# Kernel tuning notes

Hardware: AMD Instinct MI355X
Metric: run time of the kernel (lower is better)

Reference implementation:

```python
import jax, jax.numpy as jnp
import numpy as np

D = 1024
B, N = 4, 2048

def setup_inputs() -> dict:
    key = jax.random.key(0)
    ks = jax.random.split(key, 7)
    sc = 1.0 / np.sqrt(D)
    return {
        "x": jax.random.normal(ks[0], (B, N, D), dtype=jnp.float32),
        "wq_w": jax.random.normal(ks[1], (D, D), dtype=jnp.float32) * sc,
        "wq_b": jax.random.normal(ks[2], (D,), dtype=jnp.float32) * 0.01,
        "wk_w": jax.random.normal(ks[3], (D, D), dtype=jnp.float32) * sc,
        "wk_b": jax.random.normal(ks[4], (D,), dtype=jnp.float32) * 0.01,
        "wv_w": jax.random.normal(ks[5], (D, D), dtype=jnp.float32) * sc,
        "wv_b": jax.random.normal(ks[6], (D,), dtype=jnp.float32) * 0.01,
    }

def reference(x, wq_w, wq_b, wk_w, wk_b, wv_w, wv_b):
    # torch Linear: y = x @ W^T + b
    q = x @ wq_w.T + wq_b
    k = x @ wk_w.T + wk_b
    v = x @ wv_w.T + wv_b
    d = q.shape[-1]
    s = jnp.einsum("bid,bjd->bij", q, k) / jnp.sqrt(jnp.float32(d))
    # faithful to original: triu then transpose (zeros, NOT -inf, enter the softmax)
    t = jnp.swapaxes(jnp.triu(s), -2, -1)
    p = jax.nn.softmax(t, axis=-2)
    attn = jnp.swapaxes(jnp.triu(p), -2, -1) @ v
    return attn
```

## Files before the change

kernel.cpp:

```cpp
#include <hip/hip_runtime.h>
#include <hip/hip_fp16.h>
#include <cstdint>

typedef _Float16 half8_t __attribute__((ext_vector_type(8)));
typedef float f32x4 __attribute__((ext_vector_type(4)));

#define D_ 1024
#define B_ 4
#define N_ 2048
#define M_ (B_*N_)
#define NC_ 3072

#define OFF_WCAT  0u
#define OFF_BCAT  6291456u
#define OFF_XB    6303744u
#define OFF_Q     23080960u
#define OFF_K     39858176u
#define OFF_V     56635392u
#define OFF_ZP    73412608u
#define OFF_DEXP  74461184u
#define OFF_SV    74493952u
#define OFF_INVD  74756096u
#define OFF_CD    74788864u

__device__ __forceinline__ void gload_lds16(const void* g, void* l) {
  __builtin_amdgcn_global_load_lds(
      (const __attribute__((address_space(1))) unsigned int*)(uintptr_t)g,
      (__attribute__((address_space(3))) unsigned int*)(uintptr_t)l, 16, 0, 0);
}

__device__ __forceinline__ void stage128x64(const __half* rowbase, char* lds, int tid) {
#pragma unroll
  for (int inst = 0; inst < 4; ++inst) {
    int L  = inst * 4096 + tid * 16;
    int r  = L >> 7;
    int cb = L & 127;
    int cbs = cb ^ ((r & 7) << 4);
    gload_lds16((const char*)rowbase + (size_t)r * (D_ * 2) + cbs, lds + L);
  }
}

__device__ __forceinline__ half8_t ldsfrag(const char* lds, int row, int cbyte) {
  int b = (row << 7) + (cbyte ^ ((row & 7) << 4));
  return *reinterpret_cast<const half8_t*>(lds + b);
}

__device__ __forceinline__ void gemm128_core(const __half* Arow0, const __half* Brow0,
                                             char* As, char* Bs, f32x4 acc[4][4]) {
  const int tid  = threadIdx.x;
  const int lane = tid & 63;
  const int wave = tid >> 6;
  const int wm = wave >> 1, wn = wave & 1;
  for (int kt = 0; kt < 16; ++kt) {
    if (kt) __syncthreads();
    stage128x64(Arow0 + kt * 64, As, tid);
    stage128x64(Brow0 + kt * 64, Bs, tid);
    asm volatile("s_waitcnt vmcnt(0)" ::: "memory");
    __syncthreads();
#pragma unroll
    for (int kk = 0; kk < 2; ++kk) {
      const int cbyte = kk * 64 + (lane >> 4) * 16;
      half8_t a[4], b[4];
#pragma unroll
      for (int mf = 0; mf < 4; ++mf) a[mf] = ldsfrag(As, wm * 64 + mf * 16 + (lane & 15), cbyte);
#pragma unroll
      for (int nf = 0; nf < 4; ++nf) b[nf] = ldsfrag(Bs, wn * 64 + nf * 16 + (lane & 15), cbyte);
#pragma unroll
      for (int mf = 0; mf < 4; ++mf)
#pragma unroll
        for (int nf = 0; nf < 4; ++nf)
          acc[mf][nf] = __builtin_amdgcn_mfma_f32_16x16x32_f16(a[mf], b[nf], acc[mf][nf], 0, 0, 0);
    }
  }
}

__global__ __launch_bounds__(256) void k_prep(
    const float* __restrict__ x, const float* __restrict__ wq, const float* __restrict__ wk,
    const float* __restrict__ wv, const float* __restrict__ bq, const float* __restrict__ bk,
    const float* __restrict__ bv, __half* __restrict__ xb, __half* __restrict__ wcat,
    float* __restrict__ bcat, float* __restrict__ Zpart) {
  const int NX4 = (M_ * D_) / 4;
  const int NW4 = (D_ * D_) / 4;
  const int TOT = NX4 + 3 * NW4;
  int tid0 = blockIdx.x * 256 + threadIdx.x;
  int stride = gridDim.x * 256;
  for (int i = tid0; i < TOT; i += stride) {
    float4 f; __half* dst;
    if (i < NX4) {
      f = ((const float4*)x)[i];
      dst = xb + 4 * (size_t)i;
    } else {
      int j = i - NX4; int w = j / NW4; int o = j - w * NW4;
      const float* src = (w == 0) ? wq : (w == 1) ? wk : wv;
      f = ((const float4*)src)[o];
      dst = wcat + (size_t)w * (D_ * D_) + 4 * (size_t)o;
    }
    __half h0 = __float2half(f.x), h1 = __float2half(f.y),
           h2 = __float2half(f.z), h3 = __float2half(f.w);
    ushort4 u = { __half_as_ushort(h0), __half_as_ushort(h1),
                  __half_as_ushort(h2), __half_as_ushort(h3) };
    *((ushort4*)dst) = u;
  }
  if (tid0 < NC_)
    bcat[tid0] = (tid0 < 1024) ? bq[tid0] : (tid0 < 2048) ? bk[tid0 - 1024] : bv[tid0 - 2048];
  for (int i = tid0; i < M_ * 32; i += stride) Zpart[i] = 0.f;
}

__global__ __launch_bounds__(256) void k_qkv(
    const __half* __restrict__ xb, const __half* __restrict__ wcat,
    const float* __restrict__ bcat,
    __half* __restrict__ q, __half* __restrict__ kx, __half* __restrict__ v) {
  __shared__ __align__(16) char smem[32768];
  char* As = smem; char* Bs = smem + 16384;
  int bid = blockIdx.x;
  int bm = bid / 24, bn = bid % 24;
  f32x4 acc[4][4];
#pragma unroll
  for (int i = 0; i < 4; ++i)
#pragma unroll
    for (int j = 0; j < 4; ++j) acc[i][j] = f32x4{0.f, 0.f, 0.f, 0.f};
  gemm128_core(xb + (size_t)bm * 128 * D_, wcat + (size_t)bn * 128 * D_, As, Bs, acc);

  const int lane = threadIdx.x & 63;
  const int wave = threadIdx.x >> 6;
  const int wm = wave >> 1, wn = wave & 1;
  int sel = bn >> 3;
  __half* outp = (sel == 0) ? q : (sel == 1) ? kx : v;
#pragma unroll
  for (int nf = 0; nf < 4; ++nf) {
    int nloc = wn * 64 + nf * 16 + (lane & 15);
    float bias = bcat[bn * 128 + nloc];
    int ncol = (bn & 7) * 128 + nloc;
#pragma unroll
    for (int mf = 0; mf < 4; ++mf) {
#pragma unroll
      for (int r = 0; r < 4; ++r) {
        int m = bm * 128 + wm * 64 + mf * 16 + (lane >> 4) * 4 + r;
        outp[(size_t)m * D_ + ncol] = __float2half(acc[mf][nf][r] + bias);
      }
    }
  }
}

__global__ __launch_bounds__(256) void k_stats(
    const __half* __restrict__ q, const __half* __restrict__ kx,
    float* __restrict__ Zpart, float* __restrict__ dexp) {
  __shared__ __align__(16) char smem[32768];
  int bid = blockIdx.x;
  int b = bid / 136;
  int r = bid % 136;
  int ti = 0;
  while (r >= 16 - ti) { r -= 16 - ti; ++ti; }
  int tj = ti + r;

  f32x4 acc[4][4];
#pragma unroll
  for (int i = 0; i < 4; ++i)
#pragma unroll
    for (int j = 0; j < 4; ++j) acc[i][j] = f32x4{0.f, 0.f, 0.f, 0.f};
  const size_t base = (size_t)b * N_ * D_;
  gemm128_core(q + base + (size_t)ti * 128 * D_, kx + base + (size_t)tj * 128 * D_,
               smem, smem + 16384, acc);

  const int lane = threadIdx.x & 63;
  const int wave = threadIdx.x >> 6;
  const int wm = wave >> 1, wn = wave & 1;
  const bool offd = (tj > ti);
  const float scale = 0.03125f;
  int zrow0 = b * N_ + ti * 128;
#pragma unroll
  for (int mf = 0; mf < 4; ++mf) {
#pragma unroll
    for (int rg = 0; rg < 4; ++rg) {
      int il = wm * 64 + mf * 16 + (lane >> 4) * 4 + rg;
      float ssum = 0.f;
#pragma unroll
      for (int nf = 0; nf < 4; ++nf) {
        int jl = wn * 64 + nf * 16 + (lane & 15);
        float e = __expf(acc[mf][nf][rg] * scale);
        bool keep = offd || (jl >= il);
        if (!offd && jl == il) dexp[zrow0 + il] = e;
        ssum += keep ? e : 0.f;
      }
      ssum += __shfl_xor(ssum, 1);
      ssum += __shfl_xor(ssum, 2);
      ssum += __shfl_xor(ssum, 4);
      ssum += __shfl_xor(ssum, 8);
      if ((lane & 15) == 0)
        Zpart[(size_t)(zrow0 + il) * 32 + tj * 2 + wn] = ssum;
    }
  }
}

__global__ __launch_bounds__(256) void k_mid(
    const __half* __restrict__ v, const float* __restrict__ Zpart,
    const float* __restrict__ dexp, float* __restrict__ Sv,
    float* __restrict__ invD, float* __restrict__ cdiag) {
  int tid = blockIdx.x * 256 + threadIdx.x;
  int b = tid >> 14, c = (tid >> 10) & 15, d = tid & 1023;
  const __half* vp = v + ((size_t)(b * N_ + c * 128)) * D_ + d;
  float s = 0.f;
#pragma unroll 8
  for (int r2 = 0; r2 < 128; ++r2) s += __half2float(vp[(size_t)r2 * D_]);
  Sv[tid] = s;
  if (tid < M_) {
    float z = 0.f;
#pragma unroll
    for (int t = 0; t < 32; ++t) z += Zpart[(size_t)tid * 32 + t];
    float Dd = (float)(tid & (N_ - 1)) + z;
    float iv = 1.f / Dd;
    invD[tid] = iv;
    cdiag[tid] = dexp[tid] * iv;
  }
}

__global__ __launch_bounds__(256) void k_out(
    const __half* __restrict__ v, const float* __restrict__ Sv,
    const float* __restrict__ invD, const float* __restrict__ cdiag,
    float* __restrict__ out) {
  int tid = blockIdx.x * 256 + threadIdx.x;
  int b = tid >> 14, c = (tid >> 10) & 15, d = tid & 1023;
  float run = 0.f;
  for (int cc = 0; cc < c; ++cc) run += Sv[((b << 4) + cc) * 1024 + d];
  const __half* vp = v + ((size_t)(b * N_ + c * 128)) * D_ + d;
  float* op = out + ((size_t)(b * N_ + c * 128)) * D_ + d;
  int zi0 = b * N_ + c * 128;
#pragma unroll 4
  for (int r2 = 0; r2 < 128; ++r2) {
    float vi = __half2float(vp[(size_t)r2 * D_]);
    op[(size_t)r2 * D_] = run * invD[zi0 + r2] + cdiag[zi0 + r2] * vi;
    run += vi;
  }
}

extern "C" void kernel_launch(void* const* d_in, const int* in_sizes, int n_in,
                              void* d_out, int out_size, void* d_ws, size_t ws_size,
                              hipStream_t stream) {
  const float* x  = (const float*)d_in[0];
  const float* wq = (const float*)d_in[1];
  const float* bq = (const float*)d_in[2];
  const float* wk = (const float*)d_in[3];
  const float* bk = (const float*)d_in[4];
  const float* wv = (const float*)d_in[5];
  const float* bv = (const float*)d_in[6];
  float* out = (float*)d_out;
  char* ws = (char*)d_ws;

  __half* wcat = (__half*)(ws + OFF_WCAT);
  float*  bcat = (float*)(ws + OFF_BCAT);
  __half* xb   = (__half*)(ws + OFF_XB);
  __half* q    = (__half*)(ws + OFF_Q);
  __half* k    = (__half*)(ws + OFF_K);
  __half* v    = (__half*)(ws + OFF_V);
  float* Zpart = (float*)(ws + OFF_ZP);
  float* dexp  = (float*)(ws + OFF_DEXP);
  float* Sv    = (float*)(ws + OFF_SV);
  float* invD  = (float*)(ws + OFF_INVD);
  float* cdiag = (float*)(ws + OFF_CD);

  k_prep<<<dim3(2048), dim3(256), 0, stream>>>(x, wq, wk, wv, bq, bk, bv, xb, wcat, bcat, Zpart);
  k_qkv<<<dim3(64 * 24), dim3(256), 0, stream>>>(xb, wcat, bcat, q, k, v);
  k_stats<<<dim3(4 * 136), dim3(256), 0, stream>>>(q, k, Zpart, dexp);
  k_mid<<<dim3(256), dim3(256), 0, stream>>>(v, Zpart, dexp, Sv, invD, cdiag);
  k_out<<<dim3(256), dim3(256), 0, stream>>>(v, Sv, invD, cdiag, out);
}
```

Measured before the change: 141.7 us.

## Fuse V column sums into stats kernel, drop mid kernel, remap workgroups

Removes the separate k_mid kernel. The per-slab V column sums now run as extra workgroups of the stats kernel, and the Z normalisation is computed inside k_out from Zpart over only the valid tiles, so the Zpart zeroing in prep is no longer needed. k_out switches to 32-row slabs with vectorized 4-wide loads and stores across 256 blocks, and the QKV and stats grids get an XCD-aware block remap to improve L2 locality. The trade-off is more Sv prefix work per k_out block (up to 63 slabs) in exchange for one fewer launch and a cheaper prep pass.

New measurement: 127.7 us, median of 2. 1.11x faster.

```diff
diff --git a/kernel.cpp b/kernel.cpp
--- a/kernel.cpp
+++ b/kernel.cpp
@@ -20,8 +20,6 @@
 #define OFF_ZP    73412608u
 #define OFF_DEXP  74461184u
 #define OFF_SV    74493952u
-#define OFF_INVD  74756096u
-#define OFF_CD    74788864u
 
 __device__ __forceinline__ void gload_lds16(const void* g, void* l) {
   __builtin_amdgcn_global_load_lds(
@@ -78,7 +76,7 @@
     const float* __restrict__ x, const float* __restrict__ wq, const float* __restrict__ wk,
     const float* __restrict__ wv, const float* __restrict__ bq, const float* __restrict__ bk,
     const float* __restrict__ bv, __half* __restrict__ xb, __half* __restrict__ wcat,
-    float* __restrict__ bcat, float* __restrict__ Zpart) {
+    float* __restrict__ bcat) {
   const int NX4 = (M_ * D_) / 4;
   const int NW4 = (D_ * D_) / 4;
   const int TOT = NX4 + 3 * NW4;
@@ -103,7 +101,6 @@
   }
   if (tid0 < NC_)
     bcat[tid0] = (tid0 < 1024) ? bq[tid0] : (tid0 < 2048) ? bk[tid0 - 1024] : bv[tid0 - 2048];
-  for (int i = tid0; i < M_ * 32; i += stride) Zpart[i] = 0.f;
 }
 
 __global__ __launch_bounds__(256) void k_qkv(
@@ -113,7 +110,8 @@
   __shared__ __align__(16) char smem[32768];
   char* As = smem; char* Bs = smem + 16384;
   int bid = blockIdx.x;
-  int bm = bid / 24, bn = bid % 24;
+  int wgid = (bid & 7) * 192 + (bid >> 3);
+  int bm = wgid / 24, bn = wgid % 24;
   f32x4 acc[4][4];
 #pragma unroll
   for (int i = 0; i < 4; ++i)
@@ -142,13 +140,39 @@
   }
 }
 
-__global__ __launch_bounds__(256) void k_stats(
+__global__ __launch_bounds__(256) void k_statsv(
     const __half* __restrict__ q, const __half* __restrict__ kx,
-    float* __restrict__ Zpart, float* __restrict__ dexp) {
+    const __half* __restrict__ v,
+    float* __restrict__ Zpart, float* __restrict__ dexp, float* __restrict__ Sv) {
   __shared__ __align__(16) char smem[32768];
   int bid = blockIdx.x;
-  int b = bid / 136;
-  int r = bid % 136;
+  int tile = (bid & 7) * 84 + (bid >> 3);
+
+  if (tile >= 544) {
+    int sid = tile - 544;
+    int dg = threadIdx.x;
+    int d0 = dg * 4;
+#pragma unroll
+    for (int it = 0; it < 2; ++it) {
+      int slab = sid * 2 + it;
+      int b = slab >> 6, c = slab & 63;
+      const ushort4* vp = (const ushort4*)(v + ((size_t)(b * N_ + c * 32)) * D_ + d0);
+      f32x4 s = {0.f, 0.f, 0.f, 0.f};
+#pragma unroll 8
+      for (int r2 = 0; r2 < 32; ++r2) {
+        ushort4 u = vp[r2 * (D_ / 4)];
+        s[0] += __half2float(__ushort_as_half(u.x));
+        s[1] += __half2float(__ushort_as_half(u.y));
+        s[2] += __half2float(__ushort_as_half(u.z));
+        s[3] += __half2float(__ushort_as_half(u.w));
+      }
+      *(f32x4*)(Sv + (size_t)slab * D_ + d0) = s;
+    }
+    return;
+  }
+
+  int b = tile / 136;
+  int r = tile % 136;
   int ti = 0;
   while (r >= 16 - ti) { r -= 16 - ti; ++ti; }
   int tj = ti + r;
@@ -192,44 +216,52 @@
   }
 }
 
-__global__ __launch_bounds__(256) void k_mid(
-    const __half* __restrict__ v, const float* __restrict__ Zpart,
-    const float* __restrict__ dexp, float* __restrict__ Sv,
-    float* __restrict__ invD, float* __restrict__ cdiag) {
-  int tid = blockIdx.x * 256 + threadIdx.x;
-  int b = tid >> 14, c = (tid >> 10) & 15, d = tid & 1023;
-  const __half* vp = v + ((size_t)(b * N_ + c * 128)) * D_ + d;
-  float s = 0.f;
-#pragma unroll 8
-  for (int r2 = 0; r2 < 128; ++r2) s += __half2float(vp[(size_t)r2 * D_]);
-  Sv[tid] = s;
-  if (tid < M_) {
-    float z = 0.f;
-#pragma unroll
-    for (int t = 0; t < 32; ++t) z += Zpart[(size_t)tid * 32 + t];
-    float Dd = (float)(tid & (N_ - 1)) + z;
-    float iv = 1.f / Dd;
-    invD[tid] = iv;
-    cdiag[tid] = dexp[tid] * iv;
-  }
-}
-
 __global__ __launch_bounds__(256) void k_out(
     const __half* __restrict__ v, const float* __restrict__ Sv,
-    const float* __restrict__ invD, const float* __restrict__ cdiag,
+    const float* __restrict__ Zpart, const float* __restrict__ dexp,
     float* __restrict__ out) {
-  int tid = blockIdx.x * 256 + threadIdx.x;
-  int b = tid >> 14, c = (tid >> 10) & 15, d = tid & 1023;
-  float run = 0.f;
-  for (int cc = 0; cc < c; ++cc) run += Sv[((b << 4) + cc) * 1024 + d];
-  const __half* vp = v + ((size_t)(b * N_ + c * 128)) * D_ + d;
-  float* op = out + ((size_t)(b * N_ + c * 128)) * D_ + d;
-  int zi0 = b * N_ + c * 128;
+  __shared__ float sInv[32], sCd[32];
+  int slab = blockIdx.x;
+  int b = slab >> 6, c = slab & 63;
+  int dg = threadIdx.x;
+  int d0 = dg * 4;
+  int zi0 = b * N_ + c * 32;
+
+  if (dg < 32) {
+    int i  = c * 32 + dg;
+    int row = zi0 + dg;
+    int t0 = (i >> 7) * 2;
+    float z = 0.f;
+    for (int t = t0; t < 32; ++t) z += Zpart[(size_t)row * 32 + t];
+    float iv = 1.f / ((float)i + z);
+    sInv[dg] = iv;
+    sCd[dg]  = dexp[row] * iv;
+  }
+  __syncthreads();
+
+  f32x4 run = {0.f, 0.f, 0.f, 0.f};
+  for (int cc = 0; cc < c; ++cc) {
+    f32x4 sv = *(const f32x4*)(Sv + (size_t)((b << 6) + cc) * D_ + d0);
+    run[0] += sv[0]; run[1] += sv[1]; run[2] += sv[2]; run[3] += sv[3];
+  }
+  const ushort4* vp = (const ushort4*)(v + (size_t)zi0 * D_ + d0);
+  float* op = out + (size_t)zi0 * D_ + d0;
 #pragma unroll 4
-  for (int r2 = 0; r2 < 128; ++r2) {
-    float vi = __half2float(vp[(size_t)r2 * D_]);
-    op[(size_t)r2 * D_] = run * invD[zi0 + r2] + cdiag[zi0 + r2] * vi;
-    run += vi;
+  for (int r2 = 0; r2 < 32; ++r2) {
+    ushort4 u = vp[r2 * (D_ / 4)];
+    f32x4 vi;
+    vi[0] = __half2float(__ushort_as_half(u.x));
+    vi[1] = __half2float(__ushort_as_half(u.y));
+    vi[2] = __half2float(__ushort_as_half(u.z));
+    vi[3] = __half2float(__ushort_as_half(u.w));
+    float iv = sInv[r2], cd = sCd[r2];
+    f32x4 o;
+    o[0] = run[0] * iv + cd * vi[0];
+    o[1] = run[1] * iv + cd * vi[1];
+    o[2] = run[2] * iv + cd * vi[2];
+    o[3] = run[3] * iv + cd * vi[3];
+    *(f32x4*)(op + (size_t)r2 * D_) = o;
+    run[0] += vi[0]; run[1] += vi[1]; run[2] += vi[2]; run[3] += vi[3];
   }
 }
 
@@ -255,12 +287,9 @@
   float* Zpart = (float*)(ws + OFF_ZP);
   float* dexp  = (float*)(ws + OFF_DEXP);
   float* Sv    = (float*)(ws + OFF_SV);
-  float* invD  = (float*)(ws + OFF_INVD);
-  float* cdiag = (float*)(ws + OFF_CD);
-
-  k_prep<<<dim3(2048), dim3(256), 0, stream>>>(x, wq, wk, wv, bq, bk, bv, xb, wcat, bcat, Zpart);
+
+  k_prep<<<dim3(2048), dim3(256), 0, stream>>>(x, wq, wk, wv, bq, bk, bv, xb, wcat, bcat);
   k_qkv<<<dim3(64 * 24), dim3(256), 0, stream>>>(xb, wcat, bcat, q, k, v);
-  k_stats<<<dim3(4 * 136), dim3(256), 0, stream>>>(q, k, Zpart, dexp);
-  k_mid<<<dim3(256), dim3(256), 0, stream>>>(v, Zpart, dexp, Sv, invD, cdiag);
-  k_out<<<dim3(256), dim3(256), 0, stream>>>(v, Sv, invD, cdiag, out);
-}
+  k_statsv<<<dim3(672), dim3(256), 0, stream>>>(q, k, v, Zpart, dexp, Sv);
+  k_out<<<dim3(256), dim3(256), 0, stream>>>(v, Sv, Zpart, dexp, out);
+}
```
